# Optimization experiments

Hardware: AMD Instinct MI355X
Metric: run time of the kernel (lower is better)

The kernel has to match this reference:

```python
import jax, jax.numpy as jnp
import numpy as np

N = 100000
E = 1200000
D_IN = 64
D_OUT = 64


def setup_inputs() -> dict:
    key = jax.random.key(0)
    ks = jax.random.split(key, 12)
    s = 1.0 / np.sqrt(D_IN)
    return {
        "n_in_feats": jax.random.normal(ks[0], (N, D_IN), dtype=jnp.float32),
        "r_feats": jax.random.normal(ks[1], (D_IN,), dtype=jnp.float32),
        "src": jax.random.randint(ks[2], (E,), 0, N, dtype=jnp.int32),
        "dst": jax.random.randint(ks[3], (E,), 0, N, dtype=jnp.int32),
        "W_O": jax.random.normal(ks[4], (D_OUT, D_IN), dtype=jnp.float32) * s,
        "b_O": jax.random.normal(ks[5], (D_OUT,), dtype=jnp.float32) * s,
        "W_I": jax.random.normal(ks[6], (D_OUT, D_IN), dtype=jnp.float32) * s,
        "b_I": jax.random.normal(ks[7], (D_OUT,), dtype=jnp.float32) * s,
        "W_S": jax.random.normal(ks[8], (D_OUT, D_IN), dtype=jnp.float32) * s,
        "b_S": jax.random.normal(ks[9], (D_OUT,), dtype=jnp.float32) * s,
        "W_R": jax.random.normal(ks[10], (D_OUT, D_IN), dtype=jnp.float32) * s,
        "b_R": jax.random.normal(ks[11], (D_OUT,), dtype=jnp.float32) * s,
    }


def reference(n_in_feats, r_feats, src, dst, W_O, b_O, W_I, b_I, W_S, b_S, W_R, b_R):
    # comp_fn == 'sub': fn.u_sub_v composes src node feats with dst node feats
    comp_h = n_in_feats[src] - n_in_feats[dst]          # [E, D_IN]
    half = comp_h.shape[0] // 2
    # split linear transforms: first half (original edges) -> W_O, second -> W_I
    h_O = comp_h[:half] @ W_O.T + b_O                    # [E/2, D_OUT]
    h_I = comp_h[half:] @ W_I.T + b_I                    # [E/2, D_OUT]
    new_comp_h = jnp.concatenate([h_O, h_I], axis=0)     # [E, D_OUT]
    # copy_e + sum: scatter edge messages to destination nodes
    comp_edge = jax.ops.segment_sum(new_comp_h, dst, num_segments=n_in_feats.shape[0])
    # self loop path
    comp_h_s = n_in_feats - r_feats                      # broadcast [N, D_IN]
    n_out_feats = comp_h_s @ W_S.T + b_S + comp_edge     # [N, D_OUT]
    r_out_feats = r_feats @ W_R.T + b_R                  # [D_OUT]
    # batchnorm=False, dropout=0, activation=None -> identity
    return n_out_feats, r_out_feats
```

## Files before the change

### kernel.cpp

```cpp
#include <hip/hip_runtime.h>


#define DF 64
#define BCAP 2560
#define CPAD 16
#define NBMAX 1024
#define SCHUNK 4096
typedef _Float16 f16;
typedef f16 f16x8 __attribute__((ext_vector_type(8)));
typedef f16 f16x4 __attribute__((ext_vector_type(4)));
typedef f16 f16x2 __attribute__((ext_vector_type(2)));
typedef float f32x4 __attribute__((ext_vector_type(4)));

__global__ __launch_bounds__(512) void scatter_prep(
    const int* __restrict__ src, const int* __restrict__ dst,
    int* __restrict__ cur, unsigned int* __restrict__ pairBuf,
    int E, int half, int NB, int SB,
    const float* __restrict__ x, const float* __restrict__ r,
    f16* __restrict__ A, f16* __restrict__ ytab,
    const float* __restrict__ W_S, const float* __restrict__ W_O,
    const float* __restrict__ W_I, f16* __restrict__ Wf, int N) {
    int t = threadIdx.x;
    if ((int)blockIdx.x < SB) {
        __shared__ int cnt[NBMAX];
        int e0 = blockIdx.x * SCHUNK;
        int n = E - e0; if (n > SCHUNK) n = SCHUNK;
        for (int k = t; k < NBMAX; k += 512) cnt[k] = 0;
        __syncthreads();

        unsigned int ent[SCHUNK / 512];
        int bk[SCHUNK / 512];
        #pragma unroll
        for (int i = 0; i < SCHUNK / 512; i++) {
            int idx = t + i * 512;
            bk[i] = -1;
            if (idx < n) {
                int e = e0 + idx;
                int s = __builtin_nontemporal_load(src + e);
                int d = __builtin_nontemporal_load(dst + e);
                int key = (d << 1) | (e >= half ? 1 : 0);
                int b = key >> 8;
                ent[i] = (unsigned int)s | ((unsigned int)(key & 255) << 24);
                bk[i] = b;
                atomicAdd(&cnt[b], 1);
            }
        }
        __syncthreads();
        for (int k = t; k < NB; k += 512) {
            int c = cnt[k];
            cnt[k] = (c > 0) ? atomicAdd(&cur[k * CPAD], c) : 0;
        }
        __syncthreads();
        #pragma unroll
        for (int i = 0; i < SCHUNK / 512; i++) {
            if (bk[i] >= 0) {
                int pos = atomicAdd(&cnt[bk[i]], 1);
                if (pos < BCAP)
                    pairBuf[(size_t)bk[i] * BCAP + pos] = ent[i];
            }
        }
    } else {
        int tt = ((int)blockIdx.x - SB) * 512 + t;
        int ny = N * 32;
        if (tt < ny) {
            int v = tt >> 5, k = (tt & 31) * 2;
            float y0 = x[(size_t)v * DF + k]     - r[k];
            float y1 = x[(size_t)v * DF + k + 1] - r[k + 1];
            f16x2 p = {(f16)y0, (f16)y1};
            *(f16x2*)(A + (size_t)v * 192 + k) = p;
            if (ytab) *(f16x2*)(ytab + (size_t)v * 64 + k) = p;
        }
        if (tt < 6144) {
            int w = tt / 2048;
            int i = (tt % 2048) * 2;
            const float* W = (w == 0) ? W_S : (w == 1) ? W_O : W_I;
            f16x2 p = {(f16)W[i], (f16)W[i + 1]};
            *(f16x2*)(Wf + w * 4096 + i) = p;
        }
    }
}

__global__ __launch_bounds__(512) void sort_gather(
    unsigned int* __restrict__ pairBuf, const int* __restrict__ cur,
    int* __restrict__ deg,
    const f16* __restrict__ Y, int ystride, f16* __restrict__ A,
    int N, int M) {
    __shared__ unsigned int S[2048 + 8];
    __shared__ int cnt[256];
    __shared__ int pos[256];
    int b = blockIdx.x, t = threadIdx.x;
    if (t < 256) cnt[t] = 0;
    __syncthreads();
    int n = cur[b * CPAD];
    if (n > 2048) n = 2048;
    const unsigned int* seg = pairBuf + (size_t)b * BCAP;
    unsigned int ent[4];
    int ne = 0;
    for (int idx = t; idx < n; idx += 512) {
        unsigned int p = seg[idx];
        ent[ne++] = p;
        atomicAdd(&cnt[p >> 24], 1);
    }
    __syncthreads();
    int v = 0, incl = 0;
    if (t < 256) { v = cnt[t]; pos[t] = v; }
    __syncthreads();
    #pragma unroll
    for (int s = 1; s < 256; s <<= 1) {
        int u = 0;
        if (t < 256 && t >= s) u = pos[t - s];
        __syncthreads();
        if (t < 256) pos[t] += u;
        __syncthreads();
    }
    if (t < 256) {
        incl = pos[t];
        int key = (b << 8) + t;
        if (key < M) deg[key] = v;
    }
    __syncthreads();
    if (t < 256) pos[t] = incl - v;
    __syncthreads();
    for (int j = 0; j < ne; j++) {
        unsigned int p = ent[j];
        int loc = atomicAdd(&pos[p >> 24], 1);
        S[loc] = p & 0xFFFFFFu;
    }
    __syncthreads();
    if (t < 8) S[n + t] = 0;
    __syncthreads();

    const int wid = t >> 6, lane = t & 63;
    const int g = lane >> 4, q = lane & 15;
    const int vbase = b * 128;
    const f16x2 zz = {(f16)0.f, (f16)0.f};

    for (int i = 0; i < 8; i++) {
        int pp = wid * 8 + i;
        int v0 = vbase + 2 * pp, v1 = v0 + 1;
        if (v0 >= N) break;
        bool hasV1 = (v1 < N);
        int l0 = 4 * pp;
        int dO0 = cnt[l0], dI0 = cnt[l0 + 1];
        int dO1 = hasV1 ? cnt[l0 + 2] : 0;
        int dI1 = hasV1 ? cnt[l0 + 3] : 0;
        int s0 = pos[l0] - dO0;
        int t1 = s0 + dO0, t2 = t1 + dI0, t3 = t2 + dO1;
        int end = t3 + dI1;

        f16x2 aA0 = zz, aA1 = zz, a10 = zz, a11 = zz,
              a20 = zz, a21 = zz, a30 = zz, a31 = zz;

        int e = s0;
        for (; e + 8 <= end; e += 8) {
            int eA = e + g, eB = e + g + 4;
            int iA = (int)S[eA];
            int iB = (int)S[eB];
            const f16x2* pa = (const f16x2*)(Y + (size_t)iA * ystride + 4 * q);
            const f16x2* pb = (const f16x2*)(Y + (size_t)iB * ystride + 4 * q);
            f16x2 va0 = pa[0], va1 = pa[1];
            f16x2 vb0 = pb[0], vb1 = pb[1];
            aA0 += va0; aA1 += va1;
            a10 += (eA >= t1) ? va0 : zz;  a11 += (eA >= t1) ? va1 : zz;
            a20 += (eA >= t2) ? va0 : zz;  a21 += (eA >= t2) ? va1 : zz;
            a30 += (eA >= t3) ? va0 : zz;  a31 += (eA >= t3) ? va1 : zz;
            aA0 += vb0; aA1 += vb1;
            a10 += (eB >= t1) ? vb0 : zz;  a11 += (eB >= t1) ? vb1 : zz;
            a20 += (eB >= t2) ? vb0 : zz;  a21 += (eB >= t2) ? vb1 : zz;
            a30 += (eB >= t3) ? vb0 : zz;  a31 += (eB >= t3) ? vb1 : zz;
        }
        if (e < end) {
            int eA = e + g, eB = e + g + 4;
            bool inA = (eA < end), inB = (eB < end);
            int iA = (int)S[eA];
            int iB = (int)S[eB];
            const f16x2* pa = (const f16x2*)(Y + (size_t)iA * ystride + 4 * q);
            const f16x2* pb = (const f16x2*)(Y + (size_t)iB * ystride + 4 * q);
            f16x2 va0 = pa[0], va1 = pa[1];
            f16x2 vb0 = pb[0], vb1 = pb[1];
            aA0 += inA ? va0 : zz; aA1 += inA ? va1 : zz;
            a10 += (inA && eA >= t1) ? va0 : zz;  a11 += (inA && eA >= t1) ? va1 : zz;
            a20 += (inA && eA >= t2) ? va0 : zz;  a21 += (inA && eA >= t2) ? va1 : zz;
            a30 += (inA && eA >= t3) ? va0 : zz;  a31 += (inA && eA >= t3) ? va1 : zz;
            aA0 += inB ? vb0 : zz; aA1 += inB ? vb1 : zz;
            a10 += (inB && eB >= t1) ? vb0 : zz;  a11 += (inB && eB >= t1) ? vb1 : zz;
            a20 += (inB && eB >= t2) ? vb0 : zz;  a21 += (inB && eB >= t2) ? vb1 : zz;
            a30 += (inB && eB >= t3) ? vb0 : zz;  a31 += (inB && eB >= t3) ? vb1 : zz;
        }

        f16x2 acc[8] = {aA0, aA1, a10, a11, a20, a21, a30, a31};
        #pragma unroll
        for (int k = 0; k < 8; k++) {
            int w = __builtin_bit_cast(int, acc[k]);
            f16x2 u16 = __builtin_bit_cast(f16x2, __shfl_xor(w, 16, 64));
            acc[k] += u16;
            w = __builtin_bit_cast(int, acc[k]);
            f16x2 u32 = __builtin_bit_cast(f16x2, __shfl_xor(w, 32, 64));
            acc[k] += u32;
        }
        f16x2 d0l = acc[0] - acc[2], d0h = acc[1] - acc[3];
        f16x2 d1l = acc[2] - acc[4], d1h = acc[3] - acc[5];
        f16x2 d2l = acc[4] - acc[6], d2h = acc[5] - acc[7];
        f16x2 d3l = acc[6],          d3h = acc[7];
        f16x2 wl01 = (g == 0) ? d0l : d1l, wh01 = (g == 0) ? d0h : d1h;
        f16x2 wl23 = (g == 2) ? d2l : d3l, wh23 = (g == 2) ? d2h : d3h;
        f16x2 wl = (g < 2) ? wl01 : wl23,  wh = (g < 2) ? wh01 : wh23;

        int vtgt = (g < 2) ? v0 : v1;
        int voff = (g & 1) ? 128 : 64;
        float d01 = (g == 0) ? (float)dO0 : (float)dI0;
        float d23 = (g == 2) ? (float)dO1 : (float)dI1;
        float dd = (g < 2) ? d01 : d23;
        if (vtgt < N) {
            const f16x2* yp = (const f16x2*)(Y + (size_t)vtgt * ystride + 4 * q);
            f16x2 y0 = yp[0], y1 = yp[1];
            f16x4 res;
            res[0] = (f16)((float)wl[0] - dd * (float)y0[0]);
            res[1] = (f16)((float)wl[1] - dd * (float)y0[1]);
            res[2] = (f16)((float)wh[0] - dd * (float)y1[0]);
            res[3] = (f16)((float)wh[1] - dd * (float)y1[1]);
            *(f16x4*)(A + (size_t)vtgt * 192 + voff + 4 * q) = res;
        }
    }
}

__global__ __launch_bounds__(256) void gemv_mfma(const f16* __restrict__ A,
                                                 const f16* __restrict__ Wf,
                                                 const int* __restrict__ deg,
                                                 const float* __restrict__ b_O,
                                                 const float* __restrict__ b_I,
                                                 const float* __restrict__ b_S,
                                                 const float* __restrict__ r,
                                                 const float* __restrict__ W_R,
                                                 const float* __restrict__ b_R,
                                                 float* __restrict__ out,
                                                 int N, int nTiles) {
    if (blockIdx.x == 0 && threadIdx.x < 64) {
        int j = threadIdx.x;
        float s = b_R[j];
        #pragma unroll 16
        for (int k = 0; k < 64; k++) s += r[k] * W_R[j * 64 + k];
        out[(size_t)N * DF + j] = s;
    }
    int gw = (blockIdx.x * 256 + threadIdx.x) >> 6;
    int nw = gridDim.x * 4;
    const int lane = threadIdx.x & 63;
    const int mlane = lane & 15;
    const int koff = (lane >> 4) * 8;

    for (int tile = gw; tile < nTiles; tile += nw) {
        const int vbase = tile * 16;
        int va = vbase + mlane; if (va >= N) va = N - 1;
        const f16* arow = A + (size_t)va * 192 + koff;
        f16x8 af[6];
        #pragma unroll
        for (int s = 0; s < 6; s++) af[s] = *(const f16x8*)(arow + s * 32);

        f32x4 accs[4];
        #pragma unroll
        for (int c = 0; c < 4; c++) {
            f32x4 acc = {0.f, 0.f, 0.f, 0.f};
            #pragma unroll
            for (int s = 0; s < 6; s++) {
                int k = s * 32 + koff;
                const f16* bp = Wf + (k >> 6) * 4096 + (c * 16 + mlane) * 64 + (k & 63);
                f16x8 bf = *(const f16x8*)bp;
                acc = __builtin_amdgcn_mfma_f32_16x16x32_f16(af[s], bf, acc, 0, 0, 0);
            }
            accs[c] = acc;
        }

        const int mrow0 = (lane >> 4) * 4;
        #pragma unroll
        for (int reg = 0; reg < 4; reg++) {
            int v = vbase + mrow0 + reg;
            if (v >= N) continue;
            float cO = (float)deg[2 * v], cI = (float)deg[2 * v + 1];
            #pragma unroll
            for (int c = 0; c < 4; c++) {
                int j = c * 16 + mlane;
                out[(size_t)v * DF + j] = accs[c][reg] + b_S[j] + cO * b_O[j] + cI * b_I[j];
            }
        }
    }
}

extern "C" void kernel_launch(void* const* d_in, const int* in_sizes, int n_in,
                              void* d_out, int out_size, void* d_ws, size_t ws_size,
                              hipStream_t stream) {
    const float* x   = (const float*)d_in[0];
    const float* r   = (const float*)d_in[1];
    const int*   src = (const int*)d_in[2];
    const int*   dst = (const int*)d_in[3];
    const float* W_O = (const float*)d_in[4];
    const float* b_O = (const float*)d_in[5];
    const float* W_I = (const float*)d_in[6];
    const float* b_I = (const float*)d_in[7];
    const float* W_S = (const float*)d_in[8];
    const float* b_S = (const float*)d_in[9];
    const float* W_R = (const float*)d_in[10];
    const float* b_R = (const float*)d_in[11];
    float* out = (float*)d_out;

    const int N = in_sizes[0] / DF;
    const int E = in_sizes[2];
    const int half = E / 2;
    const int M = 2 * N;
    const int NB = (M + 255) >> 8;

    f16* A  = (f16*)d_ws;
    f16* Wf = A + (size_t)N * 192;
    int* deg = (int*)(Wf + 3 * 4096);
    int* cur = deg + M;
    unsigned int* pairBuf = (unsigned int*)(cur + (size_t)NB * CPAD);
    f16* ytab = (f16*)(pairBuf + (size_t)NB * BCAP);
    size_t need = (size_t)((char*)(ytab + (size_t)N * 64) - (char*)d_ws);
    const bool useYtab = (ws_size >= need);
    f16* ytabArg = useYtab ? ytab : nullptr;
    const f16* Y = useYtab ? ytab : A;
    const int ystride = useYtab ? 64 : 192;

    hipMemsetAsync(cur, 0, (size_t)NB * CPAD * sizeof(int), stream);

    const int SB = (E + SCHUNK - 1) / SCHUNK;
    const int PB = (N * 32 + 511) / 512;
    scatter_prep<<<SB + PB, 512, 0, stream>>>(src, dst, cur, pairBuf,
                                              E, half, NB, SB,
                                              x, r, A, ytabArg,
                                              W_S, W_O, W_I, Wf, N);

    sort_gather<<<NB, 512, 0, stream>>>(pairBuf, cur, deg, Y, ystride, A, N, M);

    int nTiles = (N + 15) / 16;
    gemv_mfma<<<1024, 256, 0, stream>>>(A, Wf, deg, b_O, b_I, b_S,
                                        r, W_R, b_R, out, N, nTiles);
}
```

Measured before the change: 186.1 us.

## Fuse gather and MFMA GEMM into one kernel via LDS staging

Merges the sort/gather kernel with the MFMA GEMM kernel. Each wave now writes its aggregated edge features into a shared-memory tile and runs the 16-row MFMA on them directly, so the [N,192] f16 A buffer and the deg array no longer make a global-memory round trip. Degrees are read from the LDS count array, and the r_out GEMV moves into the prep kernel. The intent is to cut one launch and the global write and read of A, at the cost of about 35KB more LDS per block and therefore lower occupancy. The fallback path for a small workspace is also dropped, so ytab is now always required.

```diff
diff --git a/kernel.cpp b/kernel.cpp
--- a/kernel.cpp
+++ b/kernel.cpp
@@ -15,11 +15,13 @@
 __global__ __launch_bounds__(512) void scatter_prep(
     const int* __restrict__ src, const int* __restrict__ dst,
     int* __restrict__ cur, unsigned int* __restrict__ pairBuf,
-    int E, int half, int NB, int SB,
+    int E, int half, int NB, int SB, int PB,
     const float* __restrict__ x, const float* __restrict__ r,
-    f16* __restrict__ A, f16* __restrict__ ytab,
+    f16* __restrict__ ytab,
     const float* __restrict__ W_S, const float* __restrict__ W_O,
-    const float* __restrict__ W_I, f16* __restrict__ Wf, int N) {
+    const float* __restrict__ W_I, f16* __restrict__ Wf,
+    const float* __restrict__ W_R, const float* __restrict__ b_R,
+    float* __restrict__ out, int N) {
     int t = threadIdx.x;
     if ((int)blockIdx.x < SB) {
         __shared__ int cnt[NBMAX];
@@ -67,8 +69,7 @@
             float y0 = x[(size_t)v * DF + k]     - r[k];
             float y1 = x[(size_t)v * DF + k + 1] - r[k + 1];
             f16x2 p = {(f16)y0, (f16)y1};
-            *(f16x2*)(A + (size_t)v * 192 + k) = p;
-            if (ytab) *(f16x2*)(ytab + (size_t)v * 64 + k) = p;
+            *(f16x2*)(ytab + (size_t)v * 64 + k) = p;
         }
         if (tt < 6144) {
             int w = tt / 2048;
@@ -77,17 +78,25 @@
             f16x2 p = {(f16)W[i], (f16)W[i + 1]};
             *(f16x2*)(Wf + w * 4096 + i) = p;
         }
+        if ((int)blockIdx.x == SB + PB - 1 && t < 64) {
+            float s = b_R[t];
+            #pragma unroll 16
+            for (int k = 0; k < 64; k++) s += r[k] * W_R[t * 64 + k];
+            out[(size_t)N * DF + t] = s;
+        }
     }
 }
 
-__global__ __launch_bounds__(512) void sort_gather(
+__global__ __launch_bounds__(512) void sort_gather_gemv(
     unsigned int* __restrict__ pairBuf, const int* __restrict__ cur,
-    int* __restrict__ deg,
-    const f16* __restrict__ Y, int ystride, f16* __restrict__ A,
+    const f16* __restrict__ Y, const f16* __restrict__ Wf,
+    const float* __restrict__ b_O, const float* __restrict__ b_I,
+    const float* __restrict__ b_S, float* __restrict__ out,
     int N, int M) {
     __shared__ unsigned int S[2048 + 8];
     __shared__ int cnt[256];
     __shared__ int pos[256];
+    __shared__ f16 T[8][16][136];
     int b = blockIdx.x, t = threadIdx.x;
     if (t < 256) cnt[t] = 0;
     __syncthreads();
@@ -113,11 +122,7 @@
         if (t < 256) pos[t] += u;
         __syncthreads();
     }
-    if (t < 256) {
-        incl = pos[t];
-        int key = (b << 8) + t;
-        if (key < M) deg[key] = v;
-    }
+    if (t < 256) incl = pos[t];
     __syncthreads();
     if (t < 256) pos[t] = incl - v;
     __syncthreads();
@@ -156,8 +161,8 @@
             int eA = e + g, eB = e + g + 4;
             int iA = (int)S[eA];
             int iB = (int)S[eB];
-            const f16x2* pa = (const f16x2*)(Y + (size_t)iA * ystride + 4 * q);
-            const f16x2* pb = (const f16x2*)(Y + (size_t)iB * ystride + 4 * q);
+            const f16x2* pa = (const f16x2*)(Y + ((size_t)iA << 6) + 4 * q);
+            const f16x2* pb = (const f16x2*)(Y + ((size_t)iB << 6) + 4 * q);
             f16x2 va0 = pa[0], va1 = pa[1];
             f16x2 vb0 = pb[0], vb1 = pb[1];
             aA0 += va0; aA1 += va1;
@@ -174,8 +179,8 @@
             bool inA = (eA < end), inB = (eB < end);
             int iA = (int)S[eA];
             int iB = (int)S[eB];
-            const f16x2* pa = (const f16x2*)(Y + (size_t)iA * ystride + 4 * q);
-            const f16x2* pb = (const f16x2*)(Y + (size_t)iB * ystride + 4 * q);
+            const f16x2* pa = (const f16x2*)(Y + ((size_t)iA << 6) + 4 * q);
+            const f16x2* pb = (const f16x2*)(Y + ((size_t)iB << 6) + 4 * q);
             f16x2 va0 = pa[0], va1 = pa[1];
             f16x2 vb0 = pb[0], vb1 = pb[1];
             aA0 += inA ? va0 : zz; aA1 += inA ? va1 : zz;
@@ -207,54 +212,34 @@
         f16x2 wl = (g < 2) ? wl01 : wl23,  wh = (g < 2) ? wh01 : wh23;
 
         int vtgt = (g < 2) ? v0 : v1;
-        int voff = (g & 1) ? 128 : 64;
         float d01 = (g == 0) ? (float)dO0 : (float)dI0;
         float d23 = (g == 2) ? (float)dO1 : (float)dI1;
         float dd = (g < 2) ? d01 : d23;
         if (vtgt < N) {
-            const f16x2* yp = (const f16x2*)(Y + (size_t)vtgt * ystride + 4 * q);
+            const f16x2* yp = (const f16x2*)(Y + ((size_t)vtgt << 6) + 4 * q);
             f16x2 y0 = yp[0], y1 = yp[1];
             f16x4 res;
             res[0] = (f16)((float)wl[0] - dd * (float)y0[0]);
             res[1] = (f16)((float)wl[1] - dd * (float)y0[1]);
             res[2] = (f16)((float)wh[0] - dd * (float)y1[0]);
             res[3] = (f16)((float)wh[1] - dd * (float)y1[1]);
-            *(f16x4*)(A + (size_t)vtgt * 192 + voff + 4 * q) = res;
-        }
-    }
-}
-
-__global__ __launch_bounds__(256) void gemv_mfma(const f16* __restrict__ A,
-                                                 const f16* __restrict__ Wf,
-                                                 const int* __restrict__ deg,
-                                                 const float* __restrict__ b_O,
-                                                 const float* __restrict__ b_I,
-                                                 const float* __restrict__ b_S,
-                                                 const float* __restrict__ r,
-                                                 const float* __restrict__ W_R,
-                                                 const float* __restrict__ b_R,
-                                                 float* __restrict__ out,
-                                                 int N, int nTiles) {
-    if (blockIdx.x == 0 && threadIdx.x < 64) {
-        int j = threadIdx.x;
-        float s = b_R[j];
-        #pragma unroll 16
-        for (int k = 0; k < 64; k++) s += r[k] * W_R[j * 64 + k];
-        out[(size_t)N * DF + j] = s;
-    }
-    int gw = (blockIdx.x * 256 + threadIdx.x) >> 6;
-    int nw = gridDim.x * 4;
-    const int lane = threadIdx.x & 63;
+            int row = 2 * i + (g >> 1);
+            int col = (g & 1) * 64 + 4 * q;
+            *(f16x4*)&T[wid][row][col] = res;
+        }
+    }
+
     const int mlane = lane & 15;
     const int koff = (lane >> 4) * 8;
-
-    for (int tile = gw; tile < nTiles; tile += nw) {
-        const int vbase = tile * 16;
-        int va = vbase + mlane; if (va >= N) va = N - 1;
-        const f16* arow = A + (size_t)va * 192 + koff;
+    const int vtile = vbase + wid * 16;
+    if (vtile < N) {
+        int va = vtile + mlane; if (va >= N) va = N - 1;
         f16x8 af[6];
-        #pragma unroll
-        for (int s = 0; s < 6; s++) af[s] = *(const f16x8*)(arow + s * 32);
+        af[0] = *(const f16x8*)(Y + ((size_t)va << 6) + koff);
+        af[1] = *(const f16x8*)(Y + ((size_t)va << 6) + 32 + koff);
+        #pragma unroll
+        for (int s = 2; s < 6; s++)
+            af[s] = *(const f16x8*)&T[wid][mlane][(s - 2) * 32 + koff];
 
         f32x4 accs[4];
         #pragma unroll
@@ -273,13 +258,15 @@
         const int mrow0 = (lane >> 4) * 4;
         #pragma unroll
         for (int reg = 0; reg < 4; reg++) {
-            int v = vbase + mrow0 + reg;
-            if (v >= N) continue;
-            float cO = (float)deg[2 * v], cI = (float)deg[2 * v + 1];
+            int vl = wid * 16 + mrow0 + reg;
+            int vv = vbase + vl;
+            if (vv >= N) continue;
+            int lk = 4 * (vl >> 1) + 2 * (vl & 1);
+            float cO = (float)cnt[lk], cI = (float)cnt[lk + 1];
             #pragma unroll
             for (int c = 0; c < 4; c++) {
                 int j = c * 16 + mlane;
-                out[(size_t)v * DF + j] = accs[c][reg] + b_S[j] + cO * b_O[j] + cI * b_I[j];
+                out[(size_t)vv * DF + j] = accs[c][reg] + b_S[j] + cO * b_O[j] + cI * b_I[j];
             }
         }
     }
@@ -308,30 +295,21 @@
     const int M = 2 * N;
     const int NB = (M + 255) >> 8;
 
-    f16* A  = (f16*)d_ws;
-    f16* Wf = A + (size_t)N * 192;
-    int* deg = (int*)(Wf + 3 * 4096);
-    int* cur = deg + M;
+    f16* Wf = (f16*)d_ws;
+    f16* ytab = Wf + 3 * 4096;
+    int* cur = (int*)(ytab + (size_t)N * 64);
     unsigned int* pairBuf = (unsigned int*)(cur + (size_t)NB * CPAD);
-    f16* ytab = (f16*)(pairBuf + (size_t)NB * BCAP);
-    size_t need = (size_t)((char*)(ytab + (size_t)N * 64) - (char*)d_ws);
-    const bool useYtab = (ws_size >= need);
-    f16* ytabArg = useYtab ? ytab : nullptr;
-    const f16* Y = useYtab ? ytab : A;
-    const int ystride = useYtab ? 64 : 192;
 
     hipMemsetAsync(cur, 0, (size_t)NB * CPAD * sizeof(int), stream);
 
     const int SB = (E + SCHUNK - 1) / SCHUNK;
     const int PB = (N * 32 + 511) / 512;
     scatter_prep<<<SB + PB, 512, 0, stream>>>(src, dst, cur, pairBuf,
-                                              E, half, NB, SB,
-                                              x, r, A, ytabArg,
-                                              W_S, W_O, W_I, Wf, N);
-
-    sort_gather<<<NB, 512, 0, stream>>>(pairBuf, cur, deg, Y, ystride, A, N, M);
-
-    int nTiles = (N + 15) / 16;
-    gemv_mfma<<<1024, 256, 0, stream>>>(A, Wf, deg, b_O, b_I, b_S,
-                                        r, W_R, b_R, out, N, nTiles);
+                                              E, half, NB, SB, PB,
+                                              x, r, ytab,
+                                              W_S, W_O, W_I, Wf,
+                                              W_R, b_R, out, N);
+
+    sort_gather_gemv<<<NB, 512, 0, stream>>>(pairBuf, cur, ytab, Wf,
+                                             b_O, b_I, b_S, out, N, M);
 }
```

Measured after the change: 186.5 us. No clear change (+0.2%).
